# Kernel optimization log

Hardware: AMD Instinct MI355X
Metric: run time of the kernel (lower is better)

The kernel has to match this reference:

```python
import jax, jax.numpy as jnp
import numpy as np

# LIF constants from norse.LIFParameters in the module
DT = 1e-3
TAU_MEM_INV = 4.0      # 1 / tau_mem, tau_mem = 0.25
TAU_SYN_INV = 200.0    # norse default 1/5e-3
V_TH = 0.1
ALPHA = 50.0           # super-spike surrogate slope
NHEAD = 4

@jax.custom_vjp
def spike(x):
    # SuperSpike: heaviside forward, surrogate gradient backward
    return (x > 0).astype(x.dtype)

def _spike_fwd(x):
    return spike(x), x

def _spike_bwd(x, g):
    return (g / (ALPHA * jnp.abs(x) + 1.0) ** 2,)

spike.defvjp(_spike_fwd, _spike_bwd)

def lif_reservoir(x, Win, Wres):
    # x: [B,S,I] -> spikes z: [B,S,R]. All batches start from zero state,
    # so the per-batch python loop of the original vectorizes over B.
    inp = jnp.einsum('bsi,ir->bsr', x, Win)  # precompute input currents
    B, S, R = inp.shape

    def step(carry, cur):  # cur: [B,R]
        v, i, z = carry
        total = cur + z @ Wres  # z=0 at t=0, matching the t>0 branch
        v_dec = v + DT * TAU_MEM_INV * (-v + i)  # v_leak = 0
        i_dec = i * (1.0 - DT * TAU_SYN_INV)
        z_new = spike(v_dec - V_TH)
        v_new = (1.0 - z_new) * v_dec            # v_reset = 0
        i_new = i_dec + total
        return (v_new, i_new, z_new), z_new

    init = (jnp.zeros((B, R), x.dtype),) * 3
    _, zs = jax.lax.scan(step, init, jnp.swapaxes(inp, 0, 1))
    return jnp.swapaxes(zs, 0, 1)  # [B,S,R]

def layer_norm(x, g, b, eps=1e-5):
    m = x.mean(-1, keepdims=True)
    v = ((x - m) ** 2).mean(-1, keepdims=True)
    return (x - m) / jnp.sqrt(v + eps) * g + b

def encoder_layer(x, Wqkv, bqkv, Wo, bo, g1, b1, g2, b2, W1, c1, W2, c2):
    # Post-norm TransformerEncoderLayer, relu activation, dropout=eval(0)
    B, S, D = x.shape
    dh = D // NHEAD
    qkv = x @ Wqkv.T + bqkv
    q, k, v = jnp.split(qkv, 3, axis=-1)
    rh = lambda t: t.reshape(B, S, NHEAD, dh)
    q, k, v = rh(q), rh(k), rh(v)
    scores = jnp.einsum('bqhd,bkhd->bhqk', q, k) / jnp.sqrt(jnp.asarray(dh, x.dtype))
    attn = jax.nn.softmax(scores, axis=-1)
    o = jnp.einsum('bhqk,bkhd->bqhd', attn, v).reshape(B, S, D)
    o = o @ Wo.T + bo
    x = layer_norm(x + o, g1, b1)
    ff = jax.nn.relu(x @ W1.T + c1) @ W2.T + c2
    return layer_norm(x + ff, g2, b2)

def setup_inputs() -> dict:
    key = jax.random.key(0)
    B, S, I, R, D, L, FF = 32, 1024, 8, 512, 256, 2, 1024
    ks = jax.random.split(key, 16)
    x = jax.random.normal(ks[0], (B, S, I), jnp.float32)
    Win = jax.random.normal(ks[1], (I, R), jnp.float32) * 0.1
    # sparse reservoir: density 0.2, values uniform [0,1)
    mask = (jax.random.uniform(ks[2], (R, R)) < 0.2).astype(jnp.float32)
    Wres = jax.random.uniform(ks[3], (R, R), jnp.float32) * mask
    Wread = jax.random.normal(ks[4], (D, R), jnp.float32) * 0.04
    bread = jnp.zeros((D,), jnp.float32)
    Wqkv = jax.random.normal(ks[5], (L, 3 * D, D), jnp.float32) * 0.05
    bqkv = jnp.zeros((L, 3 * D), jnp.float32)
    Wo = jax.random.normal(ks[6], (L, D, D), jnp.float32) * 0.05
    bo = jnp.zeros((L, D), jnp.float32)
    ln1_g = jnp.ones((L, D), jnp.float32)
    ln1_b = jnp.zeros((L, D), jnp.float32)
    ln2_g = jnp.ones((L, D), jnp.float32)
    ln2_b = jnp.zeros((L, D), jnp.float32)
    Wff1 = jax.random.normal(ks[7], (L, FF, D), jnp.float32) * 0.05
    bff1 = jnp.zeros((L, FF), jnp.float32)
    Wff2 = jax.random.normal(ks[8], (L, D, FF), jnp.float32) * 0.05
    bff2 = jnp.zeros((L, D), jnp.float32)
    return dict(x=x, Win=Win, Wres=Wres, Wread=Wread, bread=bread,
                Wqkv=Wqkv, bqkv=bqkv, Wo=Wo, bo=bo,
                ln1_g=ln1_g, ln1_b=ln1_b, ln2_g=ln2_g, ln2_b=ln2_b,
                Wff1=Wff1, bff1=bff1, Wff2=Wff2, bff2=bff2)

def reference(x, Win, Wres, Wread, bread, Wqkv, bqkv, Wo, bo,
              ln1_g, ln1_b, ln2_g, ln2_b, Wff1, bff1, Wff2, bff2):
    z = lif_reservoir(x, Win, Wres)          # [B,S,R] spike trains
    h = z @ Wread.T + bread                  # readout to transformer_dim
    for l in range(Wqkv.shape[0]):           # fixed small num_layers
        h = encoder_layer(h, Wqkv[l], bqkv[l], Wo[l], bo[l],
                          ln1_g[l], ln1_b[l], ln2_g[l], ln2_b[l],
                          Wff1[l], bff1[l], Wff2[l], bff2[l])
    return h
```

## Files before the change

kernel.cpp:

```cpp
#include <hip/hip_runtime.h>
#include <stdint.h>

using short8  = __attribute__((ext_vector_type(8))) short;
using floatx4 = __attribute__((ext_vector_type(4))) float;

typedef unsigned short u16;
typedef unsigned int u32;
typedef unsigned long long u64;

#define AS1(p) ((const __attribute__((address_space(1))) void*)(p))
#define AS3(p) ((__attribute__((address_space(3))) void*)(p))

__device__ __forceinline__ float bs2f(u16 u) { return __uint_as_float(((u32)u) << 16); }
__device__ __forceinline__ u16 f2bs(float f) {
  u32 x = __float_as_uint(f);
  x += 0x7FFFu + ((x >> 16) & 1u);
  return (u16)(x >> 16);
}
__device__ __forceinline__ float lo16(u32 u) { return __uint_as_float(u << 16); }
__device__ __forceinline__ float hi16(u32 u) { return __uint_as_float(u & 0xFFFF0000u); }

__global__ __launch_bounds__(256) void cvt_all_k(
    const float* __restrict__ s0, const float* __restrict__ s1,
    const float* __restrict__ s2, const float* __restrict__ s3,
    const float* __restrict__ s4, u16* __restrict__ d0, u16* __restrict__ d1,
    u16* __restrict__ d2, u16* __restrict__ d3, u16* __restrict__ d4) {
  const int i = blockIdx.x * 256 + threadIdx.x;
  if (i < 131072)        d0[i] = f2bs(s0[i]);
  else if (i < 524288)   d1[i - 131072] = f2bs(s1[i - 131072]);
  else if (i < 655360)   d2[i - 524288] = f2bs(s2[i - 524288]);
  else if (i < 1179648)  d3[i - 655360] = f2bs(s3[i - 655360]);
  else                   d4[i - 1179648] = f2bs(s4[i - 1179648]);
}

__global__ __launch_bounds__(512) void inp_k(const float* __restrict__ x,
                                             const float* __restrict__ Win,
                                             float* __restrict__ inp) {
  const int row = blockIdx.x;
  const int r = threadIdx.x;
  const float* xr = x + (size_t)row * 8;
  float s = 0.f;
#pragma unroll
  for (int k = 0; k < 8; ++k) s = fmaf(Win[k * 512 + r], xr[k], s);
  const int c = r >> 3, j = r & 7;
  const int idx = (j < 4) ? (c * 4 + j) : (256 + c * 4 + (j - 4));
  inp[(size_t)row * 512 + idx] = s;
}

__global__ __launch_bounds__(64, 1) void reservoir_k(
    const float* __restrict__ inp,
    const float* __restrict__ Wres,
    u16* __restrict__ zout)
{
  const int b = blockIdx.x;
  const int c = threadIdx.x & 63;
  __shared__ __align__(16) float s_in[2][4096];
  const float* ib = inp + (size_t)b * 524288;
  u16* zb = zout + (size_t)b * 524288 + c * 8;
  float v[8] = {}, ci[8] = {}, rec[8] = {};
  u32 pz = 0;
#pragma unroll
  for (int i = 0; i < 16; ++i)
    __builtin_amdgcn_global_load_lds(AS1(ib + i * 256 + c * 4),
                                     AS3(&s_in[0][i * 256 + c * 4]), 16, 0, 0);
#pragma unroll
  for (int i = 0; i < 16; ++i)
    __builtin_amdgcn_global_load_lds(AS1(ib + 4096 + i * 256 + c * 4),
                                     AS3(&s_in[1][i * 256 + c * 4]), 16, 0, 0);
  for (int g = 0; g < 128; ++g) {
    const int buf = g & 1;
    if (g < 126) __builtin_amdgcn_s_waitcnt(0x4F70);
    else         __builtin_amdgcn_s_waitcnt(0x0F70);
    asm volatile("" ::: "memory");
#pragma unroll
    for (int u = 0; u < 8; ++u) {
      const int t = g * 8 + u;
      const float4 xa = *(const float4*)&s_in[buf][u * 512 + c * 4];
      const float4 xc = *(const float4*)&s_in[buf][u * 512 + 256 + c * 4];
      const float in[8] = {xa.x, xa.y, xa.z, xa.w, xc.x, xc.y, xc.z, xc.w};
      u32 nzb = 0;
      u32 zw[4];
#pragma unroll
      for (int j = 0; j < 8; ++j) {
        const float vdec = __fadd_rn(v[j], __fmul_rn(0.004f, __fadd_rn(-v[j], ci[j])));
        const int zc = (__fadd_rn(vdec, -0.1f) > 0.f) ? 1 : 0;
        v[j] = zc ? 0.f : vdec;
        nzb |= (u32)zc << j;
        ci[j] = __fadd_rn(__fmul_rn(ci[j], 0.8f), __fadd_rn(in[j], rec[j]));
        if (j & 1) zw[j >> 1] |= zc ? 0x3F800000u : 0u;
        else       zw[j >> 1]  = zc ? 0x3F80u : 0u;
      }
      *(uint4*)(zb + (size_t)t * 512) = make_uint4(zw[0], zw[1], zw[2], zw[3]);
      const u64 anyt = __ballot((nzb ^ pz) != 0);
      if (anyt) {
#pragma unroll
        for (int j = 0; j < 8; ++j) {
          const u64 nm = __ballot((nzb >> j) & 1);
          const u64 pm = __ballot((pz >> j) & 1);
          u64 on   = nm & ~pm;
          u64 offm = pm & ~nm;
          while (on) {
            const int cc = __builtin_ctzll(on); on &= on - 1;
            const float* wr = Wres + ((size_t)(cc * 8 + j) << 9) + c * 8;
            const float4 w0 = *(const float4*)wr;
            const float4 w1 = *(const float4*)(wr + 4);
            rec[0] += w0.x; rec[1] += w0.y; rec[2] += w0.z; rec[3] += w0.w;
            rec[4] += w1.x; rec[5] += w1.y; rec[6] += w1.z; rec[7] += w1.w;
          }
          while (offm) {
            const int cc = __builtin_ctzll(offm); offm &= offm - 1;
            const float* wr = Wres + ((size_t)(cc * 8 + j) << 9) + c * 8;
            const float4 w0 = *(const float4*)wr;
            const float4 w1 = *(const float4*)(wr + 4);
            rec[0] -= w0.x; rec[1] -= w0.y; rec[2] -= w0.z; rec[3] -= w0.w;
            rec[4] -= w1.x; rec[5] -= w1.y; rec[6] -= w1.z; rec[7] -= w1.w;
          }
        }
      }
      pz = nzb;
    }
    asm volatile("" ::: "memory");
    if (g + 2 < 128) {
      const float* gt = ib + (size_t)(g + 2) * 4096;
#pragma unroll
      for (int i = 0; i < 16; ++i)
        __builtin_amdgcn_global_load_lds(AS1(gt + i * 256 + c * 4),
                                         AS3(&s_in[buf][i * 256 + c * 4]), 16, 0, 0);
    }
  }
}

enum { MODE_BF16 = 0, MODE_F32 = 1, MODE_DUAL = 2, MODE_QKV = 3 };

template <int WM, int WN, int MODE>
__global__ __launch_bounds__(WM * WN * 64) void gemm_bt(
    const u16* __restrict__ A, const u16* __restrict__ B,
    const float* __restrict__ bias, void* __restrict__ C0,
    void* __restrict__ C1, void* __restrict__ C2, int K, int lda, int ldb,
    int ldc, long long sA, long long sB, long long sC, float scale, int relu)
{
  constexpr int BM = WM * 64, BN = WN * 64, BK = 32;
  constexpr int NT = WM * WN * 64;
  constexpr int CA = BM * 4 / NT, CB = BN * 4 / NT;
  __shared__ __align__(16) u16 As[BM * BK];
  __shared__ __align__(16) u16 Bs[BN * BK];
  const int tid = threadIdx.x;
  const int bz = blockIdx.z;
  const u16* Ab = A + (size_t)bz * sA + (size_t)blockIdx.y * BM * lda;
  const u16* Bb = B + (size_t)bz * sB + (size_t)blockIdx.x * BN * ldb;
  const int wavei = tid >> 6, lane = tid & 63;
  const int r16 = lane & 15, quad = lane >> 4;
  const int wm = (wavei % WM) * 64, wn = (wavei / WM) * 64;
  floatx4 acc[4][4] = {};
  for (int k0 = 0; k0 < K; k0 += BK) {
#pragma unroll
    for (int c = 0; c < CA; ++c) {
      const int idx = c * NT + tid;
      const int row = idx >> 2, kc = (idx & 3) << 3;
      __builtin_amdgcn_global_load_lds(AS1(Ab + (size_t)row * lda + k0 + kc),
                                       AS3(As + idx * 8), 16, 0, 0);
    }
#pragma unroll
    for (int c = 0; c < CB; ++c) {
      const int idx = c * NT + tid;
      const int row = idx >> 2, kc = (idx & 3) << 3;
      __builtin_amdgcn_global_load_lds(AS1(Bb + (size_t)row * ldb + k0 + kc),
                                       AS3(Bs + idx * 8), 16, 0, 0);
    }
    __syncthreads();
    short8 af[4], bfr[4];
#pragma unroll
    for (int i = 0; i < 4; ++i)
      af[i] = *(const short8*)&As[(wm + i * 16 + r16) * BK + quad * 8];
#pragma unroll
    for (int i = 0; i < 4; ++i)
      bfr[i] = *(const short8*)&Bs[(wn + i * 16 + r16) * BK + quad * 8];
#pragma unroll
    for (int i = 0; i < 4; ++i)
#pragma unroll
      for (int j = 0; j < 4; ++j)
        acc[i][j] = __builtin_amdgcn_mfma_f32_16x16x32_bf16(af[i], bfr[j], acc[i][j], 0, 0, 0);
    __syncthreads();
  }
#pragma unroll
  for (int i = 0; i < 4; ++i) {
#pragma unroll
    for (int j = 0; j < 4; ++j) {
#pragma unroll
      for (int q = 0; q < 4; ++q) {
        const int m = blockIdx.y * BM + wm + i * 16 + quad * 4 + q;
        const int n = blockIdx.x * BN + wn + j * 16 + r16;
        float val = acc[i][j][q] * scale;
        if (bias) val += bias[n];
        if (relu) val = fmaxf(val, 0.f);
        if constexpr (MODE == MODE_BF16) {
          ((u16*)C0)[(size_t)bz * sC + (size_t)m * ldc + n] = f2bs(val);
        } else if constexpr (MODE == MODE_F32) {
          ((float*)C0)[(size_t)m * ldc + n] = val;
        } else if constexpr (MODE == MODE_DUAL) {
          ((float*)C0)[(size_t)m * ldc + n] = val;
          ((u16*)C1)[(size_t)m * ldc + n] = f2bs(val);
        } else if constexpr (MODE == MODE_QKV) {
          const int b = m >> 10, s = m & 1023;
          const u16 outv = f2bs(val);
          const int h = (n & 255) >> 6, d = n & 63;
          if (n < 256)
            ((u16*)C0)[(((size_t)(b * 4 + h)) * 1024 + s) * 64 + d] = outv;
          else if (n < 512)
            ((u16*)C1)[(((size_t)(b * 4 + h)) * 1024 + s) * 64 + d] = outv;
          else
            ((u16*)C2)[(((size_t)(b * 4 + h)) * 64 + d) * 1024 + s] = outv;
        }
      }
    }
  }
}

__global__ __launch_bounds__(256) void attn_k(
    const u16* __restrict__ q_s,
    const u16* __restrict__ k_s,
    const u16* __restrict__ v_t,
    u16* __restrict__ o16)
{
  constexpr int LQ = 72, LV = 136, LP = 136;
  __shared__ __align__(16) u16 Qs[128 * LQ];
  __shared__ __align__(16) u16 Ks[128 * LQ];
  __shared__ __align__(16) u16 Vt[64 * LV];
  __shared__ __align__(16) u16 Ps[128 * LP];
  const int tid = threadIdx.x;
  const int w = tid >> 6, lane = tid & 63;
  const int r16 = lane & 15, quad = lane >> 4;
  const int p = blockIdx.y;
  const int q0 = blockIdx.x * 128;
  const u16* qg = q_s + ((size_t)p * 1024 + q0) * 64;
  const u16* kg = k_s + (size_t)p * 65536;
  const u16* vg = v_t + (size_t)p * 65536;

#pragma unroll
  for (int it = 0; it < 4; ++it) {
    const int idx = it * 256 + tid;
    const int row = idx >> 3, c8 = (idx & 7) * 8;
    *(uint4*)&Qs[row * LQ + c8] = *(const uint4*)(qg + (size_t)row * 64 + c8);
    *(uint4*)&Ks[row * LQ + c8] = *(const uint4*)(kg + (size_t)row * 64 + c8);
  }
#pragma unroll
  for (int it = 0; it < 4; ++it) {
    const int idx = it * 256 + tid;
    const int row = idx >> 4, c8 = (idx & 15) * 8;
    *(uint4*)&Vt[row * LV + c8] = *(const uint4*)(vg + (size_t)row * 1024 + c8);
  }
  __syncthreads();

  short8 aq[2][2];
#pragma unroll
  for (int i = 0; i < 2; ++i)
#pragma unroll
    for (int kc = 0; kc < 2; ++kc)
      aq[i][kc] = *(const short8*)&Qs[(w * 32 + i * 16 + r16) * LQ + kc * 32 + quad * 8];

  floatx4 o[2][4] = {};
  float mr[2][4], l[2][4];
#pragma unroll
  for (int i = 0; i < 2; ++i)
#pragma unroll
    for (int q = 0; q < 4; ++q) { mr[i][q] = -3e38f; l[i][q] = 0.f; }

  for (int kt = 0; kt < 8; ++kt) {
    uint4 kpre[4], vpre[4];
    if (kt < 7) {
      const u16* kgn = kg + (size_t)(kt + 1) * 128 * 64;
#pragma unroll
      for (int it = 0; it < 4; ++it) {
        const int idx = it * 256 + tid;
        kpre[it] = *(const uint4*)(kgn + (size_t)(idx >> 3) * 64 + (idx & 7) * 8);
        vpre[it] = *(const uint4*)(vg + (size_t)(idx >> 4) * 1024 + (kt + 1) * 128 + (idx & 15) * 8);
      }
    }
    floatx4 s[2][8] = {};
#pragma unroll
    for (int kc = 0; kc < 2; ++kc) {
#pragma unroll
      for (int f = 0; f < 8; ++f) {
        const short8 bk = *(const short8*)&Ks[(f * 16 + r16) * LQ + kc * 32 + quad * 8];
#pragma unroll
        for (int i = 0; i < 2; ++i)
          s[i][f] = __builtin_amdgcn_mfma_f32_16x16x32_bf16(aq[i][kc], bk, s[i][f], 0, 0, 0);
      }
    }
#pragma unroll
    for (int i = 0; i < 2; ++i) {
      float mt[4] = {-3e38f, -3e38f, -3e38f, -3e38f};
#pragma unroll
      for (int f = 0; f < 8; ++f)
#pragma unroll
        for (int q = 0; q < 4; ++q) {
          s[i][f][q] *= 0.125f;
          mt[q] = fmaxf(mt[q], s[i][f][q]);
        }
#pragma unroll
      for (int off = 8; off > 0; off >>= 1)
#pragma unroll
        for (int q = 0; q < 4; ++q) mt[q] = fmaxf(mt[q], __shfl_xor(mt[q], off));
      float al[4], rs[4] = {};
#pragma unroll
      for (int q = 0; q < 4; ++q) {
        const float mn = fmaxf(mr[i][q], mt[q]);
        al[q] = __expf(mr[i][q] - mn);
        mr[i][q] = mn;
      }
#pragma unroll
      for (int f = 0; f < 8; ++f)
#pragma unroll
        for (int q = 0; q < 4; ++q) {
          const float pv = __expf(s[i][f][q] - mr[i][q]);
          s[i][f][q] = pv;
          rs[q] += pv;
        }
#pragma unroll
      for (int off = 8; off > 0; off >>= 1)
#pragma unroll
        for (int q = 0; q < 4; ++q) rs[q] += __shfl_xor(rs[q], off);
#pragma unroll
      for (int q = 0; q < 4; ++q) l[i][q] = l[i][q] * al[q] + rs[q];
#pragma unroll
      for (int n = 0; n < 4; ++n)
#pragma unroll
        for (int q = 0; q < 4; ++q) o[i][n][q] *= al[q];
#pragma unroll
      for (int f = 0; f < 8; ++f)
#pragma unroll
        for (int q = 0; q < 4; ++q)
          Ps[(w * 32 + i * 16 + quad * 4 + q) * LP + f * 16 + r16] = f2bs(s[i][f][q]);
    }
#pragma unroll
    for (int kc = 0; kc < 4; ++kc) {
      short8 ap[2];
#pragma unroll
      for (int i = 0; i < 2; ++i)
        ap[i] = *(const short8*)&Ps[(w * 32 + i * 16 + r16) * LP + kc * 32 + quad * 8];
#pragma unroll
      for (int n = 0; n < 4; ++n) {
        const short8 bv = *(const short8*)&Vt[(n * 16 + r16) * LV + kc * 32 + quad * 8];
#pragma unroll
        for (int i = 0; i < 2; ++i)
          o[i][n] = __builtin_amdgcn_mfma_f32_16x16x32_bf16(ap[i], bv, o[i][n], 0, 0, 0);
      }
    }
    __syncthreads();
    if (kt < 7) {
#pragma unroll
      for (int it = 0; it < 4; ++it) {
        const int idx = it * 256 + tid;
        *(uint4*)&Ks[(idx >> 3) * LQ + (idx & 7) * 8] = kpre[it];
        *(uint4*)&Vt[(idx >> 4) * LV + (idx & 15) * 8] = vpre[it];
      }
      __syncthreads();
    }
  }
  const int bb = p >> 2, hh = p & 3;
#pragma unroll
  for (int i = 0; i < 2; ++i)
#pragma unroll
    for (int q = 0; q < 4; ++q) {
      const float inv = 1.f / l[i][q];
      const int srow = q0 + w * 32 + i * 16 + quad * 4 + q;
#pragma unroll
      for (int n = 0; n < 4; ++n)
        o16[((size_t)bb * 1024 + srow) * 256 + hh * 64 + n * 16 + r16] =
            f2bs(o[i][n][q] * inv);
    }
}

__global__ __launch_bounds__(256) void ln_k(const float* __restrict__ x,
                                            const float* __restrict__ add,
                                            const float* __restrict__ g,
                                            const float* __restrict__ bta,
                                            float* __restrict__ y32,
                                            u16* __restrict__ y16) {
  const int row = blockIdx.x * 4 + (threadIdx.x >> 6);
  const int lane = threadIdx.x & 63;
  const size_t base = (size_t)row * 256 + lane * 4;
  const float4 xv = *(const float4*)(x + base);
  const float4 av = *(const float4*)(add + base);
  float sv[4] = {xv.x + av.x, xv.y + av.y, xv.z + av.z, xv.w + av.w};
  float sum = sv[0] + sv[1] + sv[2] + sv[3];
#pragma unroll
  for (int off = 32; off > 0; off >>= 1) sum += __shfl_xor(sum, off);
  const float mean = sum * (1.f / 256.f);
  float var = 0.f;
  float d[4];
#pragma unroll
  for (int i = 0; i < 4; ++i) { d[i] = sv[i] - mean; var += d[i] * d[i]; }
#pragma unroll
  for (int off = 32; off > 0; off >>= 1) var += __shfl_xor(var, off);
  var *= (1.f / 256.f);
  const float inv = 1.f / sqrtf(var + 1e-5f);
  float yv[4];
#pragma unroll
  for (int i = 0; i < 4; ++i)
    yv[i] = d[i] * inv * g[lane * 4 + i] + bta[lane * 4 + i];
  if (y32) *(float4*)(y32 + base) = make_float4(yv[0], yv[1], yv[2], yv[3]);
  if (y16) {
    const u32 p0 = (u32)f2bs(yv[0]) | ((u32)f2bs(yv[1]) << 16);
    const u32 p1 = (u32)f2bs(yv[2]) | ((u32)f2bs(yv[3]) << 16);
    *(uint2*)(y16 + base) = make_uint2(p0, p1);
  }
}

extern "C" void kernel_launch(void* const* d_in, const int* in_sizes, int n_in,
                              void* d_out, int out_size, void* d_ws,
                              size_t ws_size, hipStream_t stream) {
  (void)in_sizes; (void)n_in; (void)out_size; (void)ws_size;
  const float* x     = (const float*)d_in[0];
  const float* Win   = (const float*)d_in[1];
  const float* Wres  = (const float*)d_in[2];
  const float* Wread = (const float*)d_in[3];
  const float* bread = (const float*)d_in[4];
  const float* Wqkv  = (const float*)d_in[5];
  const float* bqkv  = (const float*)d_in[6];
  const float* Wo    = (const float*)d_in[7];
  const float* bo    = (const float*)d_in[8];
  const float* g1    = (const float*)d_in[9];
  const float* b1    = (const float*)d_in[10];
  const float* g2    = (const float*)d_in[11];
  const float* b2    = (const float*)d_in[12];
  const float* W1    = (const float*)d_in[13];
  const float* c1    = (const float*)d_in[14];
  const float* W2    = (const float*)d_in[15];
  const float* c2    = (const float*)d_in[16];

  char* ws = (char*)d_ws;
  size_t off = 0;
  auto carve = [&](size_t bytes) {
    char* p = ws + off;
    off += (bytes + 255) & ~(size_t)255;
    return p;
  };
  u16* z      = (u16*)carve((size_t)32 * 1024 * 512 * 2);
  u16* wrd16  = (u16*)carve((size_t)256 * 512 * 2);
  u16* wqkv16 = (u16*)carve((size_t)2 * 768 * 256 * 2);
  u16* wo16   = (u16*)carve((size_t)2 * 256 * 256 * 2);
  u16* w116   = (u16*)carve((size_t)2 * 1024 * 256 * 2);
  u16* w216   = (u16*)carve((size_t)2 * 256 * 1024 * 2);
  u16* q_s    = (u16*)carve((size_t)128 * 1024 * 64 * 2);
  u16* k_s    = (u16*)carve((size_t)128 * 1024 * 64 * 2);
  u16* v_t    = (u16*)carve((size_t)128 * 64 * 1024 * 2);
  float* h32  = (float*)carve((size_t)32768 * 256 * 4);
  float* lin  = (float*)carve((size_t)32768 * 256 * 4);
  u16* h16    = (u16*)carve((size_t)32768 * 256 * 2);
  u16* ff1    = (u16*)carve((size_t)32768 * 1024 * 2);
  u16* o16    = h16;
  float* inp  = (float*)ff1;

  cvt_all_k<<<dim3(6656), dim3(256), 0, stream>>>(Wread, Wqkv, Wo, W1, W2,
                                                  wrd16, wqkv16, wo16, w116,
                                                  w216);
  inp_k<<<dim3(32768), dim3(512), 0, stream>>>(x, Win, inp);
  reservoir_k<<<dim3(32), dim3(64), 0, stream>>>(inp, Wres, z);

  gemm_bt<2, 2, MODE_DUAL><<<dim3(2, 256, 1), dim3(256), 0, stream>>>(
      z, wrd16, bread, h32, h16, nullptr, 512, 512, 512, 256, 0, 0, 0, 1.0f, 0);

  for (int l = 0; l < 2; ++l) {
    gemm_bt<2, 2, MODE_QKV><<<dim3(6, 256, 1), dim3(256), 0, stream>>>(
        h16, wqkv16 + (size_t)l * 196608, bqkv + l * 768, q_s, k_s, v_t, 256,
        256, 256, 0, 0, 0, 0, 1.0f, 0);
    attn_k<<<dim3(8, 128), dim3(256), 0, stream>>>(q_s, k_s, v_t, o16);
    gemm_bt<2, 2, MODE_F32><<<dim3(2, 256, 1), dim3(256), 0, stream>>>(
        o16, wo16 + (size_t)l * 65536, bo + l * 256, lin, nullptr, nullptr,
        256, 256, 256, 256, 0, 0, 0, 1.0f, 0);
    ln_k<<<dim3(8192), dim3(256), 0, stream>>>(h32, lin, g1 + l * 256,
                                               b1 + l * 256, h32, h16);
    gemm_bt<2, 2, MODE_BF16><<<dim3(8, 256, 1), dim3(256), 0, stream>>>(
        h16, w116 + (size_t)l * 262144, c1 + l * 1024, ff1, nullptr, nullptr,
        256, 256, 256, 1024, 0, 0, 0, 1.0f, 1);
    gemm_bt<2, 2, MODE_F32><<<dim3(2, 256, 1), dim3(256), 0, stream>>>(
        ff1, w216 + (size_t)l * 262144, c2 + l * 256, lin, nullptr, nullptr,
        1024, 1024, 1024, 256, 0, 0, 0, 1.0f, 0);
    float* y32 = (l == 1) ? (float*)d_out : h32;
    u16* y16 = (l == 1) ? nullptr : h16;
    ln_k<<<dim3(8192), dim3(256), 0, stream>>>(h32, lin, g2 + l * 256,
                                               b2 + l * 256, y32, y16);
  }
}
```

Before: 1.373 ms.

## Fuse output/FF2 projections with residual add and LayerNorm into one GEMM kernel

Adds a gemm_ln_k kernel whose 64x256 tile covers full rows, so it can add the bias and residual and apply LayerNorm in the epilogue. This replaces the separate f32 GEMM plus ln_k pair for both LayerNorms in each layer and drops the intermediate lin buffer round trip through memory. It also folds the softmax scale and log2(e) into Q at the QKV GEMM epilogue so attention can call exp2f without a per-score multiply. The fused GEMM has no double buffering and runs only 512 blocks, which may cost some GEMM efficiency. It computes variance in a single pass as E[x^2]-mean^2, which is less numerically robust.

```diff
diff --git a/kernel.cpp b/kernel.cpp
--- a/kernel.cpp
+++ b/kernel.cpp
@@ -17,8 +17,6 @@
   x += 0x7FFFu + ((x >> 16) & 1u);
   return (u16)(x >> 16);
 }
-__device__ __forceinline__ float lo16(u32 u) { return __uint_as_float(u << 16); }
-__device__ __forceinline__ float hi16(u32 u) { return __uint_as_float(u & 0xFFFF0000u); }
 
 __global__ __launch_bounds__(256) void cvt_all_k(
     const float* __restrict__ s0, const float* __restrict__ s1,
@@ -202,18 +200,118 @@
           ((u16*)C1)[(size_t)m * ldc + n] = f2bs(val);
         } else if constexpr (MODE == MODE_QKV) {
           const int b = m >> 10, s = m & 1023;
-          const u16 outv = f2bs(val);
           const int h = (n & 255) >> 6, d = n & 63;
-          if (n < 256)
-            ((u16*)C0)[(((size_t)(b * 4 + h)) * 1024 + s) * 64 + d] = outv;
-          else if (n < 512)
-            ((u16*)C1)[(((size_t)(b * 4 + h)) * 1024 + s) * 64 + d] = outv;
-          else
-            ((u16*)C2)[(((size_t)(b * 4 + h)) * 64 + d) * 1024 + s] = outv;
+          if (n < 256) {
+            val *= 0.18033688f;
+            ((u16*)C0)[(((size_t)(b * 4 + h)) * 1024 + s) * 64 + d] = f2bs(val);
+          } else if (n < 512) {
+            ((u16*)C1)[(((size_t)(b * 4 + h)) * 1024 + s) * 64 + d] = f2bs(val);
+          } else {
+            ((u16*)C2)[(((size_t)(b * 4 + h)) * 64 + d) * 1024 + s] = f2bs(val);
+          }
         }
       }
     }
   }
+}
+
+__global__ __launch_bounds__(256) void gemm_ln_k(
+    const u16* __restrict__ A, const u16* __restrict__ B,
+    const float* __restrict__ bias, const float* __restrict__ res,
+    const float* __restrict__ gamma, const float* __restrict__ beta,
+    float* __restrict__ y32, u16* __restrict__ y16, int K)
+{
+  constexpr int BM = 64, BN = 256, BK = 32, NT = 256;
+  __shared__ __align__(16) u16 As[BM * BK];
+  __shared__ __align__(16) u16 Bs[BN * BK];
+  __shared__ float rsum[64][4];
+  __shared__ float rsq[64][4];
+  const int tid = threadIdx.x;
+  const u16* Ab = A + (size_t)blockIdx.y * BM * K;
+  const int wavei = tid >> 6, lane = tid & 63;
+  const int r16 = lane & 15, quad = lane >> 4;
+  const int wn = wavei * 64;
+  floatx4 acc[4][4] = {};
+  for (int k0 = 0; k0 < K; k0 += BK) {
+    {
+      const int row = tid >> 2, kc = (tid & 3) << 3;
+      __builtin_amdgcn_global_load_lds(AS1(Ab + (size_t)row * K + k0 + kc),
+                                       AS3(As + tid * 8), 16, 0, 0);
+    }
+#pragma unroll
+    for (int c = 0; c < 4; ++c) {
+      const int idx = c * NT + tid;
+      const int row = idx >> 2, kc = (idx & 3) << 3;
+      __builtin_amdgcn_global_load_lds(AS1(B + (size_t)row * K + k0 + kc),
+                                       AS3(Bs + idx * 8), 16, 0, 0);
+    }
+    __syncthreads();
+    short8 af[4], bfr[4];
+#pragma unroll
+    for (int i = 0; i < 4; ++i)
+      af[i] = *(const short8*)&As[(i * 16 + r16) * BK + quad * 8];
+#pragma unroll
+    for (int j = 0; j < 4; ++j)
+      bfr[j] = *(const short8*)&Bs[(wn + j * 16 + r16) * BK + quad * 8];
+#pragma unroll
+    for (int i = 0; i < 4; ++i)
+#pragma unroll
+      for (int j = 0; j < 4; ++j)
+        acc[i][j] = __builtin_amdgcn_mfma_f32_16x16x32_bf16(af[i], bfr[j], acc[i][j], 0, 0, 0);
+    __syncthreads();
+  }
+  float ps[4][4] = {}, pq[4][4] = {};
+#pragma unroll
+  for (int i = 0; i < 4; ++i)
+#pragma unroll
+    for (int j = 0; j < 4; ++j)
+#pragma unroll
+      for (int q = 0; q < 4; ++q) {
+        const int m = blockIdx.y * 64 + i * 16 + quad * 4 + q;
+        const int n = wn + j * 16 + r16;
+        const float val = acc[i][j][q] + bias[n] + res[(size_t)m * 256 + n];
+        acc[i][j][q] = val;
+        ps[i][q] += val;
+        pq[i][q] += val * val;
+      }
+#pragma unroll
+  for (int off = 1; off < 16; off <<= 1)
+#pragma unroll
+    for (int i = 0; i < 4; ++i)
+#pragma unroll
+      for (int q = 0; q < 4; ++q) {
+        ps[i][q] += __shfl_xor(ps[i][q], off);
+        pq[i][q] += __shfl_xor(pq[i][q], off);
+      }
+  if (r16 == 0) {
+#pragma unroll
+    for (int i = 0; i < 4; ++i)
+#pragma unroll
+      for (int q = 0; q < 4; ++q) {
+        rsum[i * 16 + quad * 4 + q][wavei] = ps[i][q];
+        rsq[i * 16 + quad * 4 + q][wavei] = pq[i][q];
+      }
+  }
+  __syncthreads();
+#pragma unroll
+  for (int i = 0; i < 4; ++i)
+#pragma unroll
+    for (int q = 0; q < 4; ++q) {
+      const int rl = i * 16 + quad * 4 + q;
+      const float4 s4 = *(const float4*)rsum[rl];
+      const float4 q4 = *(const float4*)rsq[rl];
+      const float mean = (s4.x + s4.y + s4.z + s4.w) * (1.f / 256.f);
+      const float var = (q4.x + q4.y + q4.z + q4.w) * (1.f / 256.f) - mean * mean;
+      const float inv = 1.f / sqrtf(var + 1e-5f);
+      const int m = blockIdx.y * 64 + rl;
+#pragma unroll
+      for (int j = 0; j < 4; ++j) {
+        const int n = wn + j * 16 + r16;
+        const float yv = (acc[i][j][q] - mean) * inv * gamma[n] + beta[n];
+        y32[(size_t)m * 256 + n] = yv;
+        if (y16) y16[(size_t)m * 256 + n] = f2bs(yv);
+      }
+    }
 }
 
 __global__ __launch_bounds__(256) void attn_k(
@@ -293,10 +391,7 @@
 #pragma unroll
       for (int f = 0; f < 8; ++f)
 #pragma unroll
-        for (int q = 0; q < 4; ++q) {
-          s[i][f][q] *= 0.125f;
-          mt[q] = fmaxf(mt[q], s[i][f][q]);
-        }
+        for (int q = 0; q < 4; ++q) mt[q] = fmaxf(mt[q], s[i][f][q]);
 #pragma unroll
       for (int off = 8; off > 0; off >>= 1)
 #pragma unroll
@@ -305,14 +400,14 @@
 #pragma unroll
       for (int q = 0; q < 4; ++q) {
         const float mn = fmaxf(mr[i][q], mt[q]);
-        al[q] = __expf(mr[i][q] - mn);
+        al[q] = exp2f(mr[i][q] - mn);
         mr[i][q] = mn;
       }
 #pragma unroll
       for (int f = 0; f < 8; ++f)
 #pragma unroll
         for (int q = 0; q < 4; ++q) {
-          const float pv = __expf(s[i][f][q] - mr[i][q]);
+          const float pv = exp2f(s[i][f][q] - mr[i][q]);
           s[i][f][q] = pv;
           rs[q] += pv;
         }
@@ -369,42 +464,6 @@
         o16[((size_t)bb * 1024 + srow) * 256 + hh * 64 + n * 16 + r16] =
             f2bs(o[i][n][q] * inv);
     }
-}
-
-__global__ __launch_bounds__(256) void ln_k(const float* __restrict__ x,
-                                            const float* __restrict__ add,
-                                            const float* __restrict__ g,
-                                            const float* __restrict__ bta,
-                                            float* __restrict__ y32,
-                                            u16* __restrict__ y16) {
-  const int row = blockIdx.x * 4 + (threadIdx.x >> 6);
-  const int lane = threadIdx.x & 63;
-  const size_t base = (size_t)row * 256 + lane * 4;
-  const float4 xv = *(const float4*)(x + base);
-  const float4 av = *(const float4*)(add + base);
-  float sv[4] = {xv.x + av.x, xv.y + av.y, xv.z + av.z, xv.w + av.w};
-  float sum = sv[0] + sv[1] + sv[2] + sv[3];
-#pragma unroll
-  for (int off = 32; off > 0; off >>= 1) sum += __shfl_xor(sum, off);
-  const float mean = sum * (1.f / 256.f);
-  float var = 0.f;
-  float d[4];
-#pragma unroll
-  for (int i = 0; i < 4; ++i) { d[i] = sv[i] - mean; var += d[i] * d[i]; }
-#pragma unroll
-  for (int off = 32; off > 0; off >>= 1) var += __shfl_xor(var, off);
-  var *= (1.f / 256.f);
-  const float inv = 1.f / sqrtf(var + 1e-5f);
-  float yv[4];
-#pragma unroll
-  for (int i = 0; i < 4; ++i)
-    yv[i] = d[i] * inv * g[lane * 4 + i] + bta[lane * 4 + i];
-  if (y32) *(float4*)(y32 + base) = make_float4(yv[0], yv[1], yv[2], yv[3]);
-  if (y16) {
-    const u32 p0 = (u32)f2bs(yv[0]) | ((u32)f2bs(yv[1]) << 16);
-    const u32 p1 = (u32)f2bs(yv[2]) | ((u32)f2bs(yv[3]) << 16);
-    *(uint2*)(y16 + base) = make_uint2(p0, p1);
-  }
 }
 
 extern "C" void kernel_launch(void* const* d_in, const int* in_sizes, int n_in,
@@ -446,7 +505,6 @@
   u16* k_s    = (u16*)carve((size_t)128 * 1024 * 64 * 2);
   u16* v_t    = (u16*)carve((size_t)128 * 64 * 1024 * 2);
   float* h32  = (float*)carve((size_t)32768 * 256 * 4);
-  float* lin  = (float*)carve((size_t)32768 * 256 * 4);
   u16* h16    = (u16*)carve((size_t)32768 * 256 * 2);
   u16* ff1    = (u16*)carve((size_t)32768 * 1024 * 2);
   u16* o16    = h16;
@@ -466,20 +524,16 @@
         h16, wqkv16 + (size_t)l * 196608, bqkv + l * 768, q_s, k_s, v_t, 256,
         256, 256, 0, 0, 0, 0, 1.0f, 0);
     attn_k<<<dim3(8, 128), dim3(256), 0, stream>>>(q_s, k_s, v_t, o16);
-    gemm_bt<2, 2, MODE_F32><<<dim3(2, 256, 1), dim3(256), 0, stream>>>(
-        o16, wo16 + (size_t)l * 65536, bo + l * 256, lin, nullptr, nullptr,
-        256, 256, 256, 256, 0, 0, 0, 1.0f, 0);
-    ln_k<<<dim3(8192), dim3(256), 0, stream>>>(h32, lin, g1 + l * 256,
-                                               b1 + l * 256, h32, h16);
+    gemm_ln_k<<<dim3(1, 512), dim3(256), 0, stream>>>(
+        o16, wo16 + (size_t)l * 65536, bo + l * 256, h32, g1 + l * 256,
+        b1 + l * 256, h32, h16, 256);
     gemm_bt<2, 2, MODE_BF16><<<dim3(8, 256, 1), dim3(256), 0, stream>>>(
         h16, w116 + (size_t)l * 262144, c1 + l * 1024, ff1, nullptr, nullptr,
         256, 256, 256, 1024, 0, 0, 0, 1.0f, 1);
-    gemm_bt<2, 2, MODE_F32><<<dim3(2, 256, 1), dim3(256), 0, stream>>>(
-        ff1, w216 + (size_t)l * 262144, c2 + l * 256, lin, nullptr, nullptr,
-        1024, 1024, 1024, 256, 0, 0, 0, 1.0f, 0);
     float* y32 = (l == 1) ? (float*)d_out : h32;
     u16* y16 = (l == 1) ? nullptr : h16;
-    ln_k<<<dim3(8192), dim3(256), 0, stream>>>(h32, lin, g2 + l * 256,
-                                               b2 + l * 256, y32, y16);
-  }
-}
+    gemm_ln_k<<<dim3(1, 512), dim3(256), 0, stream>>>(
+        ff1, w216 + (size_t)l * 262144, c2 + l * 256, h32, g2 + l * 256,
+        b2 + l * 256, y32, y16, 1024);
+  }
+}
```

New measurement: 1.342 ms. -2.2%, faster.
